# Performance work log

Hardware: AMD Instinct MI355X
Metric: run time of the kernel (lower is better)

The kernel has to match this reference:

```python
import jax, jax.numpy as jnp
import numpy as np

N = 1048576   # collocation points
D_IN = 2      # PDE spatial dim
H = 256       # mlp_x hidden
R0 = R1 = R2 = 64  # Tucker ranks (mlp_quad_last_shape)
NQ0 = NQ1 = 1024   # quadrature points per axis (quad_concat)
HQ = 128      # mlp_quad hidden
HC = 128      # core_mlp hidden
C_IN = 64     # core_init feature dim


def _mlp(x, W1, b1, W2, b2):
    # 2-layer MLP with tanh, standing in for the torch nn.Sequential MLPs
    return jnp.tanh(x @ W1 + b1) @ W2 + b2


def _r_func(quad_x, eq_param):
    # quadrature weight per point, shape (n_i, 1)
    return jnp.sin(jnp.pi * eq_param[0] * quad_x)


def setup_inputs() -> dict:
    key = jax.random.key(0)
    ks = jax.random.split(key, 16)

    def rn(k, shape, fan_in):
        return jax.random.normal(k, shape, dtype=jnp.float32) / np.float32(np.sqrt(fan_in))

    return {
        "input": jax.random.normal(ks[0], (N, D_IN), dtype=jnp.float32),
        "eq_param": jnp.ones((1,), jnp.float32),
        "quad_x0": jax.random.uniform(ks[1], (NQ0, 1), dtype=jnp.float32),
        "quad_x1": jax.random.uniform(ks[2], (NQ1, 1), dtype=jnp.float32),
        "core_init": jax.random.normal(ks[3], (1, C_IN), dtype=jnp.float32),
        # mlp_x: D_IN -> H -> R0
        "Wx1": rn(ks[4], (D_IN, H), D_IN), "bx1": jnp.zeros((H,), jnp.float32),
        "Wx2": rn(ks[5], (H, R0), H), "bx2": jnp.zeros((R0,), jnp.float32),
        # mlp_quad[0]: 1 -> HQ -> R1
        "Wq01": rn(ks[6], (1, HQ), 1), "bq01": jnp.zeros((HQ,), jnp.float32),
        "Wq02": rn(ks[7], (HQ, R1), HQ), "bq02": jnp.zeros((R1,), jnp.float32),
        # mlp_quad[1]: 1 -> HQ -> R2
        "Wq11": rn(ks[8], (1, HQ), 1), "bq11": jnp.zeros((HQ,), jnp.float32),
        "Wq12": rn(ks[9], (HQ, R2), HQ), "bq12": jnp.zeros((R2,), jnp.float32),
        # core_mlp: C_IN -> HC -> R0*R1*R2
        "Wc1": rn(ks[10], (C_IN, HC), C_IN), "bc1": jnp.zeros((HC,), jnp.float32),
        "Wc2": rn(ks[11], (HC, R0 * R1 * R2), HC), "bc2": jnp.zeros((R0 * R1 * R2,), jnp.float32),
    }


def reference(input, eq_param, quad_x0, quad_x1, core_init,
              Wx1, bx1, Wx2, bx2,
              Wq01, bq01, Wq02, bq02,
              Wq11, bq11, Wq12, bq12,
              Wc1, bc1, Wc2, bc2):
    # y, m = r_func(quad_x, eq_param) -> per-axis quadrature weights (n_i, 1)
    y0 = _r_func(quad_x0, eq_param)
    y1 = _r_func(quad_x1, eq_param)

    lhs = _mlp(input, Wx1, bx1, Wx2, bx2)                 # (N, R0)
    core = _mlp(core_init, Wc1, bc1, Wc2, bc2)            # (1, R0*R1*R2)
    core = core.reshape(R0, R1, R2)

    # loop axis 0: movedim(1,0) -> (R1,R0,R2), contract R1, sum quad points
    core = jnp.moveaxis(core, 1, 0)
    oq0 = y0 * _mlp(quad_x0, Wq01, bq01, Wq02, bq02)      # (NQ0, R1)
    # einsum('x...,cx->c...') then sum over c, fused:
    core = jnp.einsum('xab,cx->ab', core, oq0)            # (R0, R2)

    # loop axis 1: movedim(1,0) -> (R2,R0), contract R2, sum quad points
    core = jnp.moveaxis(core, 1, 0)
    oq1 = y1 * _mlp(quad_x1, Wq11, bq11, Wq12, bq12)      # (NQ1, R2)
    core = jnp.einsum('xa,cx->a', core, oq1)              # (R0,)

    # out = lhs @ core_out.T  (core_out is 1D -> vector output)
    return lhs @ core                                      # (N,)
```

## Files before the change

kernel.cpp:

```cpp
#include <hip/hip_runtime.h>
#include <hip/hip_bf16.h>
#include <stdint.h>

#define NPTS   1048576
#define HID    256
#define NQ     1024
#define HQ     128
#define HC     128
#define CIN    64
#define CORE_N 262144


#define TWO_LOG2E 2.885390081777927f

__device__ __forceinline__ bool sniff_bf16(const void* eq) {
    return ((const uint16_t*)eq)[0] == 0x3F80u;
}

__device__ __forceinline__ float ldv(const void* p, int i, bool b16) {
    return b16 ? __bfloat162float(((const __hip_bfloat16*)p)[i])
               : ((const float*)p)[i];
}

__device__ __forceinline__ float fast_tanh(float x) {
    float e = __builtin_amdgcn_exp2f(x * TWO_LOG2E);
    float r = __builtin_amdgcn_rcpf(e + 1.0f);
    return fmaf(-2.0f, r, 1.0f);
}

__global__ __launch_bounds__(1024) void k_small(
    const void* __restrict__ eq_param,
    const void* __restrict__ qx0, const void* __restrict__ qx1,
    const void* __restrict__ Wq01, const void* __restrict__ bq01,
    const void* __restrict__ Wq02, const void* __restrict__ bq02,
    const void* __restrict__ Wq11, const void* __restrict__ bq11,
    const void* __restrict__ Wq12, const void* __restrict__ bq12,
    const void* __restrict__ core_init,
    const void* __restrict__ Wc1, const void* __restrict__ bc1,
    float* __restrict__ ws)
{
    bool b16 = sniff_bf16(eq_param);
    int tid = threadIdx.x;
    int blk = blockIdx.x;
    if (blk == 2) {
        if (tid < HC) {
            float acc = ldv(bc1, tid, b16);
            for (int i = 0; i < CIN; ++i)
                acc = fmaf(ldv(core_init, i, b16), ldv(Wc1, i * HC + tid, b16), acc);
            ws[128 + tid] = fast_tanh(acc);
        } else if (tid < HC + 64) {
            ws[256 + (tid - HC)] = 0.0f;
        }
        return;
    }
    const void* qx = blk ? qx1 : qx0;
    const void* W1 = blk ? Wq11 : Wq01;
    const void* b1 = blk ? bq11 : bq01;
    const void* W2 = blk ? Wq12 : Wq02;
    const void* b2 = blk ? bq12 : bq02;

    __shared__ float upart[8][HQ];
    __shared__ float ypart[8];
    __shared__ float uj[HQ];
    __shared__ float Ytot;

    int j = tid & 127;
    int cs = tid >> 7;
    float w1 = ldv(W1, j, b16), b1j = ldv(b1, j, b16);
    float eq = ldv(eq_param, 0, b16);
    const float PI = 3.14159265358979323846f;

    float u = 0.f, ysum = 0.f;
    for (int c = cs * 128; c < cs * 128 + 128; ++c) {
        float q = ldv(qx, c, b16);
        float y = __sinf(PI * eq * q);
        ysum += y;
        u += y * fast_tanh(fmaf(q, w1, b1j));
    }
    upart[cs][j] = u;
    if (j == 0) ypart[cs] = ysum;
    __syncthreads();
    if (tid < HQ) {
        float s = 0.f;
        for (int k = 0; k < 8; ++k) s += upart[k][tid];
        uj[tid] = s;
        if (tid == 0) { float Y = 0.f; for (int k = 0; k < 8; ++k) Y += ypart[k]; Ytot = Y; }
    }
    __syncthreads();
    if (tid < 64) {
        float s = Ytot * ldv(b2, tid, b16);
        for (int jj = 0; jj < HQ; ++jj) s = fmaf(uj[jj], ldv(W2, jj * 64 + tid, b16), s);
        ws[blk * 64 + tid] = s;
    }
}

__device__ __forceinline__ float core_row_bf16(
    const __hip_bfloat16* __restrict__ row, const float* __restrict__ ws, int lane)
{
    int g = lane >> 3, yb = (lane & 7) * 8;
    float s1v[8], s0v[8];
    #pragma unroll
    for (int e = 0; e < 8; ++e) s1v[e] = ws[64 + yb + e];
    #pragma unroll
    for (int k = 0; k < 8; ++k) s0v[k] = ws[k * 8 + g];

    const uint4* rp = (const uint4*)row;
    float acc = 0.f;
    #pragma unroll
    for (int k = 0; k < 8; ++k) {
        uint4 v = rp[k * 64 + lane];
        uint32_t uu[4] = {v.x, v.y, v.z, v.w};
        float inner = 0.f;
        #pragma unroll
        for (int q = 0; q < 4; ++q) {
            float lo = __uint_as_float(uu[q] << 16);
            float hi = __uint_as_float(uu[q] & 0xffff0000u);
            inner = fmaf(lo, s1v[2 * q], inner);
            inner = fmaf(hi, s1v[2 * q + 1], inner);
        }
        acc = fmaf(inner, s0v[k], acc);
    }
    return acc;
}

__device__ __forceinline__ float core_row_f32(
    const float* __restrict__ row, const float* __restrict__ ws, int lane)
{
    int g = lane >> 4, yb = (lane & 15) * 4;
    float s1v[4], s0v[16];
    #pragma unroll
    for (int e = 0; e < 4; ++e) s1v[e] = ws[64 + yb + e];
    #pragma unroll
    for (int k = 0; k < 16; ++k) s0v[k] = ws[k * 4 + g];

    const float4* rp = (const float4*)row;
    float acc = 0.f;
    #pragma unroll
    for (int k = 0; k < 16; ++k) {
        float4 v = rp[k * 64 + lane];
        float inner = v.x * s1v[0];
        inner = fmaf(v.y, s1v[1], inner);
        inner = fmaf(v.z, s1v[2], inner);
        inner = fmaf(v.w, s1v[3], inner);
        acc = fmaf(inner, s0v[k], acc);
    }
    return acc;
}

__global__ __launch_bounds__(256) void k_core(
    const void* __restrict__ Wc2, const void* __restrict__ bc2,
    const void* __restrict__ eq_param,
    const float* __restrict__ ws, float* __restrict__ cacc)
{
    bool b16 = sniff_bf16(eq_param);
    int tid = threadIdx.x;
    int wave = tid >> 6, lane = tid & 63;
    int gid = blockIdx.x * 4 + wave;
    int j = gid >> 6;
    int a = gid & 63;

    const void* base = (j < HC) ? Wc2 : bc2;
    size_t off = (j < HC) ? ((size_t)j * CORE_N + (size_t)a * 4096)
                          : ((size_t)a * 4096);
    float coeff = (j < HC) ? ws[128 + j] : 1.0f;

    float acc = b16 ? core_row_bf16((const __hip_bfloat16*)base + off, ws, lane)
                    : core_row_f32((const float*)base + off, ws, lane);

    for (int offl = 32; offl > 0; offl >>= 1) acc += __shfl_down(acc, offl);
    if (lane == 0) atomicAdd(&cacc[a], acc * coeff);
}

__global__ __launch_bounds__(256) void k_prep(
    const void* __restrict__ Wx1, const void* __restrict__ bx1,
    const void* __restrict__ Wx2, const void* __restrict__ bx2,
    const void* __restrict__ eq_param,
    const float* __restrict__ cacc, float* __restrict__ ws)
{
    bool b16 = sniff_bf16(eq_param);
    __shared__ float cv[64];
    __shared__ float red[4];
    int tid = threadIdx.x;
    if (tid < 64) cv[tid] = cacc[tid];
    __syncthreads();
    float w = 0.f;
    for (int a = 0; a < 64; ++a) w = fmaf(ldv(Wx2, tid * 64 + a, b16), cv[a], w);
    float4 t;
    t.x = TWO_LOG2E * ldv(Wx1, tid, b16);
    t.y = TWO_LOG2E * ldv(Wx1, HID + tid, b16);
    t.z = TWO_LOG2E * ldv(bx1, tid, b16);
    t.w = -2.0f * w;
    ((float4*)(ws + 320))[tid] = t;

    float p = w + ((tid < 64) ? ldv(bx2, tid, b16) * cv[tid] : 0.f);
    for (int offl = 32; offl > 0; offl >>= 1) p += __shfl_down(p, offl);
    if ((tid & 63) == 0) red[tid >> 6] = p;
    __syncthreads();
    if (tid == 0) ws[1344] = red[0] + red[1] + red[2] + red[3];
}

__global__ __launch_bounds__(256) void k_main(
    const void* __restrict__ x, const void* __restrict__ eq_param,
    const float* __restrict__ ws, void* __restrict__ out)
{
    bool b16 = sniff_bf16(eq_param);
    const float4* __restrict__ tbl = (const float4*)(ws + 320);
    const int stride = NPTS / 2;
    int p0 = blockIdx.x * 256 + threadIdx.x;

    float x0[2], x1[2], acc[2];
    if (b16) {
        #pragma unroll
        for (int i = 0; i < 2; ++i) {
            uint32_t u = ((const uint32_t*)x)[p0 + i * stride];
            x0[i] = __uint_as_float(u << 16);
            x1[i] = __uint_as_float(u & 0xffff0000u);
        }
    } else {
        #pragma unroll
        for (int i = 0; i < 2; ++i) {
            float2 v = ((const float2*)x)[p0 + i * stride];
            x0[i] = v.x;
            x1[i] = v.y;
        }
    }
    float boff = ws[1344];
    acc[0] = boff; acc[1] = boff;

    #pragma unroll 4
    for (int jj = 0; jj < HID; ++jj) {
        float4 t = tbl[jj];
        #pragma unroll
        for (int i = 0; i < 2; ++i) {
            float gch = fmaf(x0[i], t.x, fmaf(x1[i], t.y, t.z));
            float e = __builtin_amdgcn_exp2f(gch);
            float r = __builtin_amdgcn_rcpf(e + 1.0f);
            acc[i] = fmaf(t.w, r, acc[i]);
        }
    }
    if (b16) {
        #pragma unroll
        for (int i = 0; i < 2; ++i)
            ((__hip_bfloat16*)out)[p0 + i * stride] = __float2bfloat16(acc[i]);
    } else {
        #pragma unroll
        for (int i = 0; i < 2; ++i)
            ((float*)out)[p0 + i * stride] = acc[i];
    }
}

extern "C" void kernel_launch(void* const* d_in, const int* in_sizes, int n_in,
                              void* d_out, int out_size, void* d_ws, size_t ws_size,
                              hipStream_t stream) {
    (void)in_sizes; (void)n_in; (void)out_size; (void)ws_size;
    const void* input     = d_in[0];
    const void* eq_param  = d_in[1];
    const void* quad_x0   = d_in[2];
    const void* quad_x1   = d_in[3];
    const void* core_init = d_in[4];
    const void* Wx1  = d_in[5];
    const void* bx1  = d_in[6];
    const void* Wx2  = d_in[7];
    const void* bx2  = d_in[8];
    const void* Wq01 = d_in[9];
    const void* bq01 = d_in[10];
    const void* Wq02 = d_in[11];
    const void* bq02 = d_in[12];
    const void* Wq11 = d_in[13];
    const void* bq11 = d_in[14];
    const void* Wq12 = d_in[15];
    const void* bq12 = d_in[16];
    const void* Wc1  = d_in[17];
    const void* bc1  = d_in[18];
    const void* Wc2  = d_in[19];
    const void* bc2  = d_in[20];

    float* ws = (float*)d_ws;

    k_small<<<3, 1024, 0, stream>>>(eq_param, quad_x0, quad_x1,
                                    Wq01, bq01, Wq02, bq02,
                                    Wq11, bq11, Wq12, bq12,
                                    core_init, Wc1, bc1, ws);
    k_core<<<(129 * 64) / 4, 256, 0, stream>>>(Wc2, bc2, eq_param, ws, ws + 256);
    k_prep<<<1, 256, 0, stream>>>(Wx1, bx1, Wx2, bx2, eq_param, ws + 256, ws);
    k_main<<<NPTS / 512, 256, 0, stream>>>(input, eq_param, ws, d_out);
}
```

Measured before the change: 358.9 us.

## Fuse prep into core via last-block reduction; share reciprocal across point pairs

Removes the separate single-block k_prep launch. The last k_core block to finish, found with an atomic counter and thread fences, now builds the per-hidden-unit table. In k_main the two points' sigmoid denominators are combined so that one rcp instruction serves both points, with the exponent clamped at 30 to avoid overflow of the product. This trims a kernel launch and halves transcendental reciprocals, at the cost of slight precision change and added atomic/fence overhead in k_core.

```diff
diff --git a/kernel.cpp b/kernel.cpp
--- a/kernel.cpp
+++ b/kernel.cpp
@@ -9,6 +9,7 @@
 #define HC     128
 #define CIN    64
 #define CORE_N 262144
+#define NBLK_CORE 2064
 
 
 #define TWO_LOG2E 2.885390081777927f
@@ -50,6 +51,8 @@
             ws[128 + tid] = fast_tanh(acc);
         } else if (tid < HC + 64) {
             ws[256 + (tid - HC)] = 0.0f;
+        } else if (tid == HC + 64) {
+            ((unsigned*)ws)[1345] = 0u;
         }
         return;
     }
@@ -150,7 +153,9 @@
 __global__ __launch_bounds__(256) void k_core(
     const void* __restrict__ Wc2, const void* __restrict__ bc2,
     const void* __restrict__ eq_param,
-    const float* __restrict__ ws, float* __restrict__ cacc)
+    const void* __restrict__ Wx1, const void* __restrict__ bx1,
+    const void* __restrict__ Wx2, const void* __restrict__ bx2,
+    float* __restrict__ ws, float* __restrict__ cacc)
 {
     bool b16 = sniff_bf16(eq_param);
     int tid = threadIdx.x;
@@ -169,22 +174,25 @@
 
     for (int offl = 32; offl > 0; offl >>= 1) acc += __shfl_down(acc, offl);
     if (lane == 0) atomicAdd(&cacc[a], acc * coeff);
-}
-
-__global__ __launch_bounds__(256) void k_prep(
-    const void* __restrict__ Wx1, const void* __restrict__ bx1,
-    const void* __restrict__ Wx2, const void* __restrict__ bx2,
-    const void* __restrict__ eq_param,
-    const float* __restrict__ cacc, float* __restrict__ ws)
-{
-    bool b16 = sniff_bf16(eq_param);
+
+    __shared__ int is_last;
     __shared__ float cv[64];
     __shared__ float red[4];
-    int tid = threadIdx.x;
-    if (tid < 64) cv[tid] = cacc[tid];
-    __syncthreads();
+    __syncthreads();
+    if (tid == 0) {
+        __threadfence();
+        unsigned v = atomicAdd((unsigned*)ws + 1345, 1u);
+        is_last = (v == NBLK_CORE - 1u);
+    }
+    __syncthreads();
+    if (!is_last) return;
+
+    __threadfence();
+    if (tid < 64) cv[tid] = atomicAdd(&cacc[tid], 0.0f);
+    __syncthreads();
+
     float w = 0.f;
-    for (int a = 0; a < 64; ++a) w = fmaf(ldv(Wx2, tid * 64 + a, b16), cv[a], w);
+    for (int aa = 0; aa < 64; ++aa) w = fmaf(ldv(Wx2, tid * 64 + aa, b16), cv[aa], w);
     float4 t;
     t.x = TWO_LOG2E * ldv(Wx1, tid, b16);
     t.y = TWO_LOG2E * ldv(Wx1, HID + tid, b16);
@@ -230,13 +238,15 @@
     #pragma unroll 4
     for (int jj = 0; jj < HID; ++jj) {
         float4 t = tbl[jj];
-        #pragma unroll
-        for (int i = 0; i < 2; ++i) {
-            float gch = fmaf(x0[i], t.x, fmaf(x1[i], t.y, t.z));
-            float e = __builtin_amdgcn_exp2f(gch);
-            float r = __builtin_amdgcn_rcpf(e + 1.0f);
-            acc[i] = fmaf(t.w, r, acc[i]);
-        }
+        float g0 = fmaf(x0[0], t.x, fmaf(x1[0], t.y, t.z));
+        float g1 = fmaf(x0[1], t.x, fmaf(x1[1], t.y, t.z));
+        g0 = __builtin_fminf(g0, 30.0f);
+        g1 = __builtin_fminf(g1, 30.0f);
+        float A = __builtin_amdgcn_exp2f(g0) + 1.0f;
+        float B = __builtin_amdgcn_exp2f(g1) + 1.0f;
+        float rP = __builtin_amdgcn_rcpf(A * B);
+        acc[0] = fmaf(t.w, B * rP, acc[0]);
+        acc[1] = fmaf(t.w, A * rP, acc[1]);
     }
     if (b16) {
         #pragma unroll
@@ -281,7 +291,7 @@
                                     Wq01, bq01, Wq02, bq02,
                                     Wq11, bq11, Wq12, bq12,
                                     core_init, Wc1, bc1, ws);
-    k_core<<<(129 * 64) / 4, 256, 0, stream>>>(Wc2, bc2, eq_param, ws, ws + 256);
-    k_prep<<<1, 256, 0, stream>>>(Wx1, bx1, Wx2, bx2, eq_param, ws + 256, ws);
+    k_core<<<NBLK_CORE, 256, 0, stream>>>(Wc2, bc2, eq_param,
+                                          Wx1, bx1, Wx2, bx2, ws, ws + 256);
     k_main<<<NPTS / 512, 256, 0, stream>>>(input, eq_param, ws, d_out);
 }
```

Measured after the change: 452.8 us. 26.2% more time.

## Batch core rows per wave, pad atomic slots, share one reciprocal across two points

Applied to the files above, without the earlier changes.

k_core now has each wave walk four Wc2 row chunks (plus the bias chunk for the first 64 waves) and accumulate them locally. This cuts the grid from 2064 to 512 blocks and reduces atomics per output slot. The atomic accumulators are spaced 32 floats apart to avoid contention on shared cache lines, and the workspace offsets move to match. In k_main, the two per-point reciprocals are replaced by one reciprocal of the product A*B, with exponents clamped at 30 to avoid overflow. This halves the rcp count in the hot loop but adds multiplies and slightly changes rounding.

```diff
diff --git a/kernel.cpp b/kernel.cpp
--- a/kernel.cpp
+++ b/kernel.cpp
@@ -49,7 +49,7 @@
                 acc = fmaf(ldv(core_init, i, b16), ldv(Wc1, i * HC + tid, b16), acc);
             ws[128 + tid] = fast_tanh(acc);
         } else if (tid < HC + 64) {
-            ws[256 + (tid - HC)] = 0.0f;
+            ws[256 + (tid - HC) * 32] = 0.0f;
         }
         return;
     }
@@ -94,21 +94,14 @@
     }
 }
 
-__device__ __forceinline__ float core_row_bf16(
-    const __hip_bfloat16* __restrict__ row, const float* __restrict__ ws, int lane)
-{
-    int g = lane >> 3, yb = (lane & 7) * 8;
-    float s1v[8], s0v[8];
-    #pragma unroll
-    for (int e = 0; e < 8; ++e) s1v[e] = ws[64 + yb + e];
-    #pragma unroll
-    for (int k = 0; k < 8; ++k) s0v[k] = ws[k * 8 + g];
-
-    const uint4* rp = (const uint4*)row;
+__device__ __forceinline__ float chunk_dot_bf16(
+    const uint4* __restrict__ rp, int lane,
+    const float* __restrict__ s0v, const float* __restrict__ s1v)
+{
     float acc = 0.f;
     #pragma unroll
-    for (int k = 0; k < 8; ++k) {
-        uint4 v = rp[k * 64 + lane];
+    for (int kk = 0; kk < 8; ++kk) {
+        uint4 v = rp[kk * 64 + lane];
         uint32_t uu[4] = {v.x, v.y, v.z, v.w};
         float inner = 0.f;
         #pragma unroll
@@ -118,31 +111,24 @@
             inner = fmaf(lo, s1v[2 * q], inner);
             inner = fmaf(hi, s1v[2 * q + 1], inner);
         }
-        acc = fmaf(inner, s0v[k], acc);
+        acc = fmaf(inner, s0v[kk], acc);
     }
     return acc;
 }
 
-__device__ __forceinline__ float core_row_f32(
-    const float* __restrict__ row, const float* __restrict__ ws, int lane)
-{
-    int g = lane >> 4, yb = (lane & 15) * 4;
-    float s1v[4], s0v[16];
-    #pragma unroll
-    for (int e = 0; e < 4; ++e) s1v[e] = ws[64 + yb + e];
-    #pragma unroll
-    for (int k = 0; k < 16; ++k) s0v[k] = ws[k * 4 + g];
-
-    const float4* rp = (const float4*)row;
+__device__ __forceinline__ float chunk_dot_f32(
+    const float4* __restrict__ rp, int lane,
+    const float* __restrict__ s0v, const float* __restrict__ s1v)
+{
     float acc = 0.f;
     #pragma unroll
-    for (int k = 0; k < 16; ++k) {
-        float4 v = rp[k * 64 + lane];
+    for (int kk = 0; kk < 16; ++kk) {
+        float4 v = rp[kk * 64 + lane];
         float inner = v.x * s1v[0];
         inner = fmaf(v.y, s1v[1], inner);
         inner = fmaf(v.z, s1v[2], inner);
         inner = fmaf(v.w, s1v[3], inner);
-        acc = fmaf(inner, s0v[k], acc);
+        acc = fmaf(inner, s0v[kk], acc);
     }
     return acc;
 }
@@ -154,21 +140,53 @@
 {
     bool b16 = sniff_bf16(eq_param);
     int tid = threadIdx.x;
-    int wave = tid >> 6, lane = tid & 63;
-    int gid = blockIdx.x * 4 + wave;
-    int j = gid >> 6;
-    int a = gid & 63;
-
-    const void* base = (j < HC) ? Wc2 : bc2;
-    size_t off = (j < HC) ? ((size_t)j * CORE_N + (size_t)a * 4096)
-                          : ((size_t)a * 4096);
-    float coeff = (j < HC) ? ws[128 + j] : 1.0f;
-
-    float acc = b16 ? core_row_bf16((const __hip_bfloat16*)base + off, ws, lane)
-                    : core_row_f32((const float*)base + off, ws, lane);
+    int lane = tid & 63;
+    int W = blockIdx.x * 4 + (tid >> 6);
+    int a = W & 63;
+    int j0 = W >> 6;
+
+    float acc = 0.f;
+    if (b16) {
+        int g = lane >> 3, yb = (lane & 7) * 8;
+        float s1v[8], s0v[8];
+        #pragma unroll
+        for (int e = 0; e < 8; ++e) s1v[e] = ws[64 + yb + e];
+        #pragma unroll
+        for (int kk = 0; kk < 8; ++kk) s0v[kk] = ws[kk * 8 + g];
+
+        const uint4* base = (const uint4*)((const __hip_bfloat16*)Wc2 + (size_t)a * 4096);
+        const size_t rowstep = CORE_N / 8;
+        #pragma unroll 2
+        for (int k = 0; k < 4; ++k) {
+            int j = j0 + 32 * k;
+            float d = chunk_dot_bf16(base + (size_t)j * rowstep, lane, s0v, s1v);
+            acc = fmaf(d, ws[128 + j], acc);
+        }
+        if (W < 64)
+            acc += chunk_dot_bf16((const uint4*)((const __hip_bfloat16*)bc2 + (size_t)a * 4096),
+                                  lane, s0v, s1v);
+    } else {
+        int g = lane >> 4, yb = (lane & 15) * 4;
+        float s1v[4], s0v[16];
+        #pragma unroll
+        for (int e = 0; e < 4; ++e) s1v[e] = ws[64 + yb + e];
+        #pragma unroll
+        for (int kk = 0; kk < 16; ++kk) s0v[kk] = ws[kk * 4 + g];
+
+        const float4* base = (const float4*)((const float*)Wc2 + (size_t)a * 4096);
+        const size_t rowstep = CORE_N / 4;
+        for (int k = 0; k < 4; ++k) {
+            int j = j0 + 32 * k;
+            float d = chunk_dot_f32(base + (size_t)j * rowstep, lane, s0v, s1v);
+            acc = fmaf(d, ws[128 + j], acc);
+        }
+        if (W < 64)
+            acc += chunk_dot_f32((const float4*)((const float*)bc2 + (size_t)a * 4096),
+                                 lane, s0v, s1v);
+    }
 
     for (int offl = 32; offl > 0; offl >>= 1) acc += __shfl_down(acc, offl);
-    if (lane == 0) atomicAdd(&cacc[a], acc * coeff);
+    if (lane == 0) atomicAdd(&cacc[a * 32], acc);
 }
 
 __global__ __launch_bounds__(256) void k_prep(
@@ -181,7 +199,7 @@
     __shared__ float cv[64];
     __shared__ float red[4];
     int tid = threadIdx.x;
-    if (tid < 64) cv[tid] = cacc[tid];
+    if (tid < 64) cv[tid] = cacc[tid * 32];
     __syncthreads();
     float w = 0.f;
     for (int a = 0; a < 64; ++a) w = fmaf(ldv(Wx2, tid * 64 + a, b16), cv[a], w);
@@ -190,13 +208,13 @@
     t.y = TWO_LOG2E * ldv(Wx1, HID + tid, b16);
     t.z = TWO_LOG2E * ldv(bx1, tid, b16);
     t.w = -2.0f * w;
-    ((float4*)(ws + 320))[tid] = t;
+    ((float4*)(ws + 2560))[tid] = t;
 
     float p = w + ((tid < 64) ? ldv(bx2, tid, b16) * cv[tid] : 0.f);
     for (int offl = 32; offl > 0; offl >>= 1) p += __shfl_down(p, offl);
     if ((tid & 63) == 0) red[tid >> 6] = p;
     __syncthreads();
-    if (tid == 0) ws[1344] = red[0] + red[1] + red[2] + red[3];
+    if (tid == 0) ws[3584] = red[0] + red[1] + red[2] + red[3];
 }
 
 __global__ __launch_bounds__(256) void k_main(
@@ -204,7 +222,7 @@
     const float* __restrict__ ws, void* __restrict__ out)
 {
     bool b16 = sniff_bf16(eq_param);
-    const float4* __restrict__ tbl = (const float4*)(ws + 320);
+    const float4* __restrict__ tbl = (const float4*)(ws + 2560);
     const int stride = NPTS / 2;
     int p0 = blockIdx.x * 256 + threadIdx.x;
 
@@ -224,19 +242,21 @@
             x1[i] = v.y;
         }
     }
-    float boff = ws[1344];
+    float boff = ws[3584];
     acc[0] = boff; acc[1] = boff;
 
     #pragma unroll 4
     for (int jj = 0; jj < HID; ++jj) {
         float4 t = tbl[jj];
-        #pragma unroll
-        for (int i = 0; i < 2; ++i) {
-            float gch = fmaf(x0[i], t.x, fmaf(x1[i], t.y, t.z));
-            float e = __builtin_amdgcn_exp2f(gch);
-            float r = __builtin_amdgcn_rcpf(e + 1.0f);
-            acc[i] = fmaf(t.w, r, acc[i]);
-        }
+        float g0 = fmaf(x0[0], t.x, fmaf(x1[0], t.y, t.z));
+        float g1 = fmaf(x0[1], t.x, fmaf(x1[1], t.y, t.z));
+        g0 = __builtin_fminf(g0, 30.0f);
+        g1 = __builtin_fminf(g1, 30.0f);
+        float A = __builtin_amdgcn_exp2f(g0) + 1.0f;
+        float B = __builtin_amdgcn_exp2f(g1) + 1.0f;
+        float rP = __builtin_amdgcn_rcpf(A * B);
+        acc[0] = fmaf(t.w, B * rP, acc[0]);
+        acc[1] = fmaf(t.w, A * rP, acc[1]);
     }
     if (b16) {
         #pragma unroll
@@ -281,7 +301,7 @@
                                     Wq01, bq01, Wq02, bq02,
                                     Wq11, bq11, Wq12, bq12,
                                     core_init, Wc1, bc1, ws);
-    k_core<<<(129 * 64) / 4, 256, 0, stream>>>(Wc2, bc2, eq_param, ws, ws + 256);
+    k_core<<<512, 256, 0, stream>>>(Wc2, bc2, eq_param, ws, ws + 256);
     k_prep<<<1, 256, 0, stream>>>(Wx1, bx1, Wx2, bx2, eq_param, ws + 256, ws);
     k_main<<<NPTS / 512, 256, 0, stream>>>(input, eq_param, ws, d_out);
 }
```

Measured after the change: 352.4 us. About the same (-1.8%).
